# Performance work log

Hardware: AMD Instinct MI355X
Metric: run time of the kernel (lower is better)

## Reference

```python
import jax, jax.numpy as jnp
import numpy as np

Q = 2.0
TEMPERATURE = 1.0
EXP = 1.0 / (Q - 1.0)  # exponent 1/(q-1); q=2 -> sparsemax-style projection
N_BISECT_ITERS = 50    # enough for xtol ~ 1e-6 over an interval of width ~ (u_max - u_min + 10)


def setup_inputs() -> dict:
    key = jax.random.key(0)
    k_x, k_w1, k_w2 = jax.random.split(key, 3)
    B, D, H, E = 8192, 4096, 256, 64
    x = jax.random.normal(k_x, (B, D), dtype=jnp.float32)
    w1 = jax.random.normal(k_w1, (D, H), dtype=jnp.float32) * 0.02
    b1 = jnp.zeros((H,), dtype=jnp.float32)
    w2 = jax.random.normal(k_w2, (H, E), dtype=jnp.float32) * 0.05
    b2 = jnp.zeros((E,), dtype=jnp.float32)
    return {"x": x, "w1": w1, "b1": b1, "w2": w2, "b2": b2}


def _bisect_tau(us):
    # us: [B, E] = utilities / temperature. Find per-row tau with sum(relu(us - tau)**EXP) = 1.
    lo = jnp.min(us, axis=-1) - 10.0   # constraint(lo) > 0
    hi = jnp.max(us, axis=-1)          # constraint(hi) = -1 < 0

    def body(i, carry):
        lo, hi = carry
        mid = 0.5 * (lo + hi)
        f = jnp.sum(jnp.maximum(us - mid[..., None], 0.0) ** EXP, axis=-1) - 1.0
        pos = f > 0.0  # constraint is decreasing in tau: root is above mid
        return (jnp.where(pos, mid, lo), jnp.where(pos, hi, mid))

    lo, hi = jax.lax.fori_loop(0, N_BISECT_ITERS, body, (lo, hi))
    return 0.5 * (lo + hi)  # [B]


def reference(x, w1, b1, w2, b2):
    # utility_net (Dropout is identity in eval mode)
    h = jax.nn.relu(x @ w1 + b1)            # [B, 256]
    utilities = h @ w2 + b2                  # [B, E]
    us = utilities / TEMPERATURE
    # tau is found by root-finding on detached values in the original (.item()),
    # so it is a constant w.r.t. differentiation.
    tau = jax.lax.stop_gradient(_bisect_tau(jax.lax.stop_gradient(us)))
    p = jnp.maximum(us - tau[..., None], 0.0) ** EXP   # [B, E]
    p = p / (jnp.sum(p, axis=-1, keepdims=True) + 1e-8)
    return p
```

## Files before the change

kernel.cpp:

```cpp
#include <hip/hip_runtime.h>
#include <stdint.h>

typedef _Float16 f16;
typedef _Float16 f16x8 __attribute__((ext_vector_type(8)));
typedef float f32x4 __attribute__((ext_vector_type(4)));

#define D_DIM 4096
#define H_DIM 256
#define E_DIM 64
#define BM 128
#define KSPLIT 4
#define NKT2 16
#define HP_SLICE (8192 * 256)

__global__ void pack_kernel(const float* __restrict__ w1, f16* __restrict__ w1s,
                            const float* __restrict__ w2, f16* __restrict__ w2s) {
  const int b = blockIdx.x;
  const int t = threadIdx.x;
  if (b < 512) {
    const int u = b * 256 + t;
    const int lane = u & 63;
    const int kk = (u >> 6) & 1;
    const int c16 = (u >> 7) & 15;
    const int kt = u >> 11;
    const int g = lane >> 4, r = lane & 15;
    const int k0 = kt * 64 + kk * 32 + g * 8;
    const int col = c16 * 16 + r;
    f16x8 o;
#pragma unroll
    for (int j = 0; j < 8; ++j) o[j] = (f16)w1[(size_t)(k0 + j) * H_DIM + col];
    *(f16x8*)(w1s + (size_t)u * 8) = o;
  } else {
    const int u = (b - 512) * 256 + t;
    const int lane = u & 63;
    const int ks = (u >> 6) & 7;
    const int cg = u >> 9;
    const int g = lane >> 4, r = lane & 15;
    const int k0 = ks * 32 + g * 8;
    const int col = cg * 16 + r;
    f16x8 o;
#pragma unroll
    for (int j = 0; j < 8; ++j) o[j] = (f16)w2[(size_t)(k0 + j) * E_DIM + col];
    *(f16x8*)(w2s + (size_t)u * 8) = o;
  }
}

__launch_bounds__(512, 2)
__global__ void gemm1_splitk_kernel(const float* __restrict__ x,
                                    const f16* __restrict__ w1s,
                                    f16* __restrict__ hpart) {
  __shared__ __align__(16) float xbuf[4][BM * 64];

  const int t = threadIdx.x;
  const int lane = t & 63;
  const int wn = t >> 6;
  const int wm = wn >> 2, wc = wn & 3;
  const int g = lane >> 4, r = lane & 15;
  const int bid = blockIdx.x;
  const int ks = bid & 3;
  const int brow = (bid >> 2) * BM;
  const int kph = (bid * 5) & 15;
#define KT(s) ((kph + (s)) & 15)

  const int drow = lane >> 4;
  int hbo[4];
#pragma unroll
  for (int i = 0; i < 4; ++i) hbo[i] = ((lane & 15) ^ ((i * 4 + drow) & 15)) * 4;
  const float* dbase = x + (size_t)(brow + wn * 16 + drow) * D_DIM + ks * 1024;

  const f16* bptr = w1s + (size_t)ks * (16 * 16384) + (size_t)(wc * 8) * 512 + lane * 8;

  f32x4 acc[4][4];
#pragma unroll
  for (int mf = 0; mf < 4; ++mf)
#pragma unroll
    for (int nf = 0; nf < 4; ++nf) acc[mf][nf] = (f32x4){0.f, 0.f, 0.f, 0.f};

  f16x8 BE[8], BO[8];

#define GLDS(bufidx, kt)                                                        \
  {                                                                             \
    _Pragma("unroll") for (int i = 0; i < 4; ++i) {                             \
      const float* gp_ = dbase + (size_t)(i * 4) * D_DIM + (kt) * 64 + hbo[i];  \
      __builtin_amdgcn_global_load_lds(                                         \
          (const __attribute__((address_space(1))) void*)gp_,                   \
          (__attribute__((address_space(3))) void*)&xbuf[bufidx][(wn * 4 + i) * 256], \
          16, 0, 0);                                                            \
    }                                                                           \
  }
#define LDB(kt, B)                                                      \
  {                                                                     \
    const f16* p_ = bptr + (size_t)(kt) * 16384;                        \
    _Pragma("unroll") for (int q = 0; q < 8; ++q)                       \
      (B)[q] = *(const f16x8*)(p_ + q * 512);                           \
  }
#define COMP(bufidx, B)                                                         \
  {                                                                             \
    _Pragma("unroll") for (int kk = 0; kk < 2; ++kk) {                          \
      _Pragma("unroll") for (int mf = 0; mf < 4; ++mf) {                        \
        const int row_ = wm * 64 + mf * 16 + r;                                 \
        const float* bp_ = &xbuf[bufidx][row_ * 64];                            \
        const int L0_ = kk * 8 + g * 2;                                         \
        const float4 a0_ = *(const float4*)(bp_ + ((L0_ ^ r) << 2));            \
        const float4 a1_ = *(const float4*)(bp_ + (((L0_ + 1) ^ r) << 2));      \
        f16x8 af_;                                                              \
        af_[0] = (f16)a0_.x; af_[1] = (f16)a0_.y;                               \
        af_[2] = (f16)a0_.z; af_[3] = (f16)a0_.w;                               \
        af_[4] = (f16)a1_.x; af_[5] = (f16)a1_.y;                               \
        af_[6] = (f16)a1_.z; af_[7] = (f16)a1_.w;                               \
        _Pragma("unroll") for (int nf = 0; nf < 4; ++nf)                        \
          acc[mf][nf] = __builtin_amdgcn_mfma_f32_16x16x32_f16(                 \
              af_, (B)[nf * 2 + kk], acc[mf][nf], 0, 0, 0);                     \
      }                                                                         \
    }                                                                           \
  }
#define STEP(s, bidx, B)                                  \
  {                                                       \
    GLDS(((s) + 2) & 3, KT((s) + 2));                     \
    asm volatile("s_waitcnt vmcnt(16)" ::: "memory");     \
    __builtin_amdgcn_s_barrier();                         \
    COMP(bidx, B);                                        \
    LDB(KT((s) + 2), B);                                  \
  }
#define STEPN(s, bidx, B, WAIT)                           \
  {                                                       \
    asm volatile(WAIT ::: "memory");                      \
    __builtin_amdgcn_s_barrier();                         \
    COMP(bidx, B);                                        \
  }

  GLDS(0, KT(0));
  LDB(KT(0), BE);
  GLDS(1, KT(1));
  LDB(KT(1), BO);

#pragma unroll 1
  for (int q = 0; q < 3; ++q) {
    const int s0 = q * 4;
    STEP(s0 + 0, 0, BE);
    STEP(s0 + 1, 1, BO);
    STEP(s0 + 2, 2, BE);
    STEP(s0 + 3, 3, BO);
  }
  STEP(12, 0, BE);
  STEP(13, 1, BO);
  STEPN(14, 2, BE, "s_waitcnt vmcnt(12)");
  STEPN(15, 3, BO, "s_waitcnt vmcnt(0)");

  f16* hp = hpart + (size_t)ks * HP_SLICE + (size_t)brow * H_DIM;
#pragma unroll
  for (int mf = 0; mf < 4; ++mf)
#pragma unroll
    for (int nf = 0; nf < 4; ++nf) {
      const int col = wc * 64 + nf * 16 + r;
#pragma unroll
      for (int j = 0; j < 4; ++j) {
        const int row = wm * 64 + mf * 16 + g * 4 + j;
        hp[(size_t)row * H_DIM + col] = (f16)acc[mf][nf][j];
      }
    }
}

__launch_bounds__(512)
__global__ void reduce_fused_kernel(const f16* __restrict__ hpart,
                                    const float* __restrict__ b1,
                                    const f16* __restrict__ w2s,
                                    const float* __restrict__ b2,
                                    float* __restrict__ out) {
  __shared__ __align__(16) char smem[24576];
  f16* h_lds = (f16*)smem;
  float* u_lds = (float*)(smem + 16384);

  const int t = threadIdx.x;
  const int lane = t & 63;
  const int wn = t >> 6;
  const int g = lane >> 4, r = lane & 15;
  const int brow = blockIdx.x * 32;

  const int row = t >> 4;
  const int col0 = (t & 15) << 4;
  const f16* base = hpart + (size_t)(brow + row) * H_DIM + col0;
  float a[16];
#pragma unroll
  for (int j = 0; j < 16; ++j) a[j] = 0.f;
#pragma unroll
  for (int c = 0; c < KSPLIT; ++c) {
    const f16x8 va = *(const f16x8*)(base + (size_t)c * HP_SLICE);
    const f16x8 vb = *(const f16x8*)(base + (size_t)c * HP_SLICE + 8);
#pragma unroll
    for (int j = 0; j < 8; ++j) { a[j] += (float)va[j]; a[8 + j] += (float)vb[j]; }
  }
  {
    const int s8 = (row & 7) << 3;
    f16x8 h0, h1;
#pragma unroll
    for (int j = 0; j < 8; ++j) {
      h0[j] = (f16)fmaxf(a[j] + b1[col0 + j], 0.f);
      h1[j] = (f16)fmaxf(a[8 + j] + b1[col0 + 8 + j], 0.f);
    }
    *(f16x8*)(h_lds + row * 256 + (col0 ^ s8)) = h0;
    *(f16x8*)(h_lds + row * 256 + ((col0 + 8) ^ s8)) = h1;
  }
  __syncthreads();

  const int rh2 = wn & 1;
  const int cg = wn >> 1;
  f32x4 acc2 = {0.f, 0.f, 0.f, 0.f};
  const f16* w2p = w2s + (size_t)(cg * 8) * 512 + lane * 8;
#pragma unroll
  for (int ksi = 0; ksi < 8; ++ksi) {
    const int arow = rh2 * 16 + r;
    const int kb = ksi * 32 + g * 8;
    const f16x8 af = *(const f16x8*)(h_lds + arow * 256 + (kb ^ ((arow & 7) << 3)));
    const f16x8 bf = *(const f16x8*)(w2p + ksi * 512);
    acc2 = __builtin_amdgcn_mfma_f32_16x16x32_f16(af, bf, acc2, 0, 0, 0);
  }
  {
    const int col = cg * 16 + r;
    const float bias = b2[col];
#pragma unroll
    for (int j = 0; j < 4; ++j) {
      const int rr = rh2 * 16 + g * 4 + j;
      u_lds[rr * 64 + col] = acc2[j] + bias;
    }
  }
  __syncthreads();

  const int srow = wn * 4 + (lane >> 4);
  const int scol = (lane & 15) << 2;
  const float4 uv = *(const float4*)(u_lds + srow * 64 + scol);
  float u0 = uv.x, u1 = uv.y, u2 = uv.z, u3 = uv.w;

  float mx = fmaxf(fmaxf(u0, u1), fmaxf(u2, u3));
  float mn = fminf(fminf(u0, u1), fminf(u2, u3));
#pragma unroll
  for (int m = 1; m < 16; m <<= 1) {
    mx = fmaxf(mx, __shfl_xor(mx, m));
    mn = fminf(mn, __shfl_xor(mn, m));
  }
  float lo = mn - 10.0f, hi = mx;
#pragma unroll 1
  for (int it = 0; it < 32; ++it) {
    const float mid = 0.5f * (lo + hi);
    float sm = fmaxf(u0 - mid, 0.f) + fmaxf(u1 - mid, 0.f) +
               fmaxf(u2 - mid, 0.f) + fmaxf(u3 - mid, 0.f);
#pragma unroll
    for (int m = 1; m < 16; m <<= 1) sm += __shfl_xor(sm, m);
    const bool pos = (sm - 1.0f) > 0.0f;
    lo = pos ? mid : lo;
    hi = pos ? hi : mid;
  }
  const float tau = 0.5f * (lo + hi);
  const float p0 = fmaxf(u0 - tau, 0.f);
  const float p1 = fmaxf(u1 - tau, 0.f);
  const float p2 = fmaxf(u2 - tau, 0.f);
  const float p3 = fmaxf(u3 - tau, 0.f);
  float sum = p0 + p1 + p2 + p3;
#pragma unroll
  for (int m = 1; m < 16; m <<= 1) sum += __shfl_xor(sum, m);
  const float inv = 1.0f / (sum + 1e-8f);
  float4 pv;
  pv.x = p0 * inv; pv.y = p1 * inv; pv.z = p2 * inv; pv.w = p3 * inv;
  *(float4*)(out + (size_t)(brow + srow) * E_DIM + scol) = pv;
}

extern "C" void kernel_launch(void* const* d_in, const int* in_sizes, int n_in,
                              void* d_out, int out_size, void* d_ws, size_t ws_size,
                              hipStream_t stream) {
  const float* x  = (const float*)d_in[0];
  const float* w1 = (const float*)d_in[1];
  const float* b1 = (const float*)d_in[2];
  const float* w2 = (const float*)d_in[3];
  const float* b2 = (const float*)d_in[4];
  float* out = (float*)d_out;

  char* wsb = (char*)d_ws;
  f16* w1s = (f16*)wsb;
  f16* w2s = (f16*)(wsb + (2u << 20));
  f16* hpart = (f16*)(wsb + (4u << 20));

  pack_kernel<<<520, 256, 0, stream>>>(w1, w1s, w2, w2s);
  gemm1_splitk_kernel<<<256, 512, 0, stream>>>(x, w1s, hpart);
  reduce_fused_kernel<<<256, 512, 0, stream>>>(hpart, b1, w2s, b2, out);
}
```

Baseline: 53.07 us.

## Stage x as fp16 in LDS and DMA W1 tiles into shared double buffers

```diff
diff --git a/kernel.cpp b/kernel.cpp
--- a/kernel.cpp
+++ b/kernel.cpp
@@ -3,6 +3,7 @@
 
 typedef _Float16 f16;
 typedef _Float16 f16x8 __attribute__((ext_vector_type(8)));
+typedef _Float16 f16x4 __attribute__((ext_vector_type(4)));
 typedef float f32x4 __attribute__((ext_vector_type(4)));
 
 #define D_DIM 4096
@@ -45,16 +46,18 @@
   }
 }
 
-__launch_bounds__(512, 2)
+__launch_bounds__(512)
 __global__ void gemm1_splitk_kernel(const float* __restrict__ x,
                                     const f16* __restrict__ w1s,
                                     f16* __restrict__ hpart) {
-  __shared__ __align__(16) float xbuf[4][BM * 64];
+  __shared__ __align__(16) f16 Abuf[2][BM * 64];
+  __shared__ __align__(16) f16 Bbuf[2][16384];
 
   const int t = threadIdx.x;
   const int lane = t & 63;
   const int wn = t >> 6;
-  const int wm = wn >> 2, wc = wn & 3;
+  const int wm = wn >> 2;
+  const int wc = wn & 3;
   const int g = lane >> 4, r = lane & 15;
   const int bid = blockIdx.x;
   const int ks = bid & 3;
@@ -62,13 +65,11 @@
   const int kph = (bid * 5) & 15;
 #define KT(s) ((kph + (s)) & 15)
 
-  const int drow = lane >> 4;
-  int hbo[4];
-#pragma unroll
-  for (int i = 0; i < 4; ++i) hbo[i] = ((lane & 15) ^ ((i * 4 + drow) & 15)) * 4;
-  const float* dbase = x + (size_t)(brow + wn * 16 + drow) * D_DIM + ks * 1024;
-
-  const f16* bptr = w1s + (size_t)ks * (16 * 16384) + (size_t)(wc * 8) * 512 + lane * 8;
+  const float* xb = x + (size_t)(brow + (t >> 4)) * D_DIM + ks * 1024 + ((t & 15) << 2);
+  const int stw_swz = (((t & 15) << 2) ^ (((t >> 4) & 7) << 3));
+  const int stw_row0 = (t >> 4);
+
+  const f16* bsl = w1s + (size_t)ks * (16 * 16384);
 
   f32x4 acc[4][4];
 #pragma unroll
@@ -76,76 +77,68 @@
 #pragma unroll
     for (int nf = 0; nf < 4; ++nf) acc[mf][nf] = (f32x4){0.f, 0.f, 0.f, 0.f};
 
-  f16x8 BE[8], BO[8];
-
-#define GLDS(bufidx, kt)                                                        \
-  {                                                                             \
-    _Pragma("unroll") for (int i = 0; i < 4; ++i) {                             \
-      const float* gp_ = dbase + (size_t)(i * 4) * D_DIM + (kt) * 64 + hbo[i];  \
-      __builtin_amdgcn_global_load_lds(                                         \
-          (const __attribute__((address_space(1))) void*)gp_,                   \
-          (__attribute__((address_space(3))) void*)&xbuf[bufidx][(wn * 4 + i) * 256], \
-          16, 0, 0);                                                            \
-    }                                                                           \
-  }
-#define LDB(kt, B)                                                      \
+  float4 xA[4];
+
+#define LDX(kt)                                                         \
   {                                                                     \
-    const f16* p_ = bptr + (size_t)(kt) * 16384;                        \
-    _Pragma("unroll") for (int q = 0; q < 8; ++q)                       \
-      (B)[q] = *(const f16x8*)(p_ + q * 512);                           \
-  }
-#define COMP(bufidx, B)                                                         \
+    _Pragma("unroll") for (int i = 0; i < 4; ++i)                       \
+      xA[i] = *(const float4*)(xb + (size_t)i * (32 * D_DIM) + (kt) * 64); \
+  }
+#define STW(p)                                                          \
+  {                                                                     \
+    _Pragma("unroll") for (int i = 0; i < 4; ++i) {                     \
+      f16x4 hv_;                                                        \
+      hv_[0] = (f16)xA[i].x; hv_[1] = (f16)xA[i].y;                     \
+      hv_[2] = (f16)xA[i].z; hv_[3] = (f16)xA[i].w;                     \
+      *(f16x4*)(&Abuf[p][(i * 32 + stw_row0) * 64 + stw_swz]) = hv_;    \
+    }                                                                   \
+  }
+#define DMAB(p, kt)                                                     \
+  {                                                                     \
+    _Pragma("unroll") for (int q = 0; q < 4; ++q) {                     \
+      const f16* gs_ = bsl + (size_t)(kt) * 16384 +                     \
+                       (q * 512 + wn * 64 + lane) * 8;                  \
+      __builtin_amdgcn_global_load_lds(                                 \
+          (const __attribute__((address_space(1))) void*)gs_,           \
+          (__attribute__((address_space(3))) void*)                     \
+              (&Bbuf[p][(q * 512 + wn * 64) * 8]),                      \
+          16, 0, 0);                                                    \
+    }                                                                   \
+  }
+#define COMP(p)                                                                 \
   {                                                                             \
     _Pragma("unroll") for (int kk = 0; kk < 2; ++kk) {                          \
+      const int kb_ = (kk * 32 + g * 8) ^ ((r & 7) << 3);                       \
       _Pragma("unroll") for (int mf = 0; mf < 4; ++mf) {                        \
         const int row_ = wm * 64 + mf * 16 + r;                                 \
-        const float* bp_ = &xbuf[bufidx][row_ * 64];                            \
-        const int L0_ = kk * 8 + g * 2;                                         \
-        const float4 a0_ = *(const float4*)(bp_ + ((L0_ ^ r) << 2));            \
-        const float4 a1_ = *(const float4*)(bp_ + (((L0_ + 1) ^ r) << 2));      \
-        f16x8 af_;                                                              \
-        af_[0] = (f16)a0_.x; af_[1] = (f16)a0_.y;                               \
-        af_[2] = (f16)a0_.z; af_[3] = (f16)a0_.w;                               \
-        af_[4] = (f16)a1_.x; af_[5] = (f16)a1_.y;                               \
-        af_[6] = (f16)a1_.z; af_[7] = (f16)a1_.w;                               \
-        _Pragma("unroll") for (int nf = 0; nf < 4; ++nf)                        \
+        const f16x8 af_ = *(const f16x8*)(&Abuf[p][row_ * 64 + kb_]);           \
+        _Pragma("unroll") for (int nf = 0; nf < 4; ++nf) {                      \
+          const f16x8 bf_ =                                                     \
+              *(const f16x8*)(&Bbuf[p][(wc * 8 + nf * 2 + kk) * 512 + lane * 8]); \
           acc[mf][nf] = __builtin_amdgcn_mfma_f32_16x16x32_f16(                 \
-              af_, (B)[nf * 2 + kk], acc[mf][nf], 0, 0, 0);                     \
+              af_, bf_, acc[mf][nf], 0, 0, 0);                                  \
+        }                                                                       \
       }                                                                         \
     }                                                                           \
   }
-#define STEP(s, bidx, B)                                  \
-  {                                                       \
-    GLDS(((s) + 2) & 3, KT((s) + 2));                     \
-    asm volatile("s_waitcnt vmcnt(16)" ::: "memory");     \
-    __builtin_amdgcn_s_barrier();                         \
-    COMP(bidx, B);                                        \
-    LDB(KT((s) + 2), B);                                  \
-  }
-#define STEPN(s, bidx, B, WAIT)                           \
-  {                                                       \
-    asm volatile(WAIT ::: "memory");                      \
-    __builtin_amdgcn_s_barrier();                         \
-    COMP(bidx, B);                                        \
-  }
-
-  GLDS(0, KT(0));
-  LDB(KT(0), BE);
-  GLDS(1, KT(1));
-  LDB(KT(1), BO);
+
+  DMAB(0, KT(0));
+  LDX(KT(0));
+  STW(0);
+  LDX(KT(1));
+  __syncthreads();
 
 #pragma unroll 1
-  for (int q = 0; q < 3; ++q) {
-    const int s0 = q * 4;
-    STEP(s0 + 0, 0, BE);
-    STEP(s0 + 1, 1, BO);
-    STEP(s0 + 2, 2, BE);
-    STEP(s0 + 3, 3, BO);
-  }
-  STEP(12, 0, BE);
-  STEP(13, 1, BO);
-  STEPN(14, 2, BE, "s_waitcnt vmcnt(12)");
-  STEPN(15, 3, BO, "s_waitcnt vmcnt(0)");
+  for (int s = 0; s < NKT2; ++s) {
+    const int p = s & 1;
+    if (s + 1 < NKT2) {
+      DMAB(p ^ 1, KT(s + 1));
+      STW(p ^ 1);
+      if (s + 2 < NKT2) LDX(KT(s + 2));
+    }
+    COMP(p);
+    __syncthreads();
+  }
 
   f16* hp = hpart + (size_t)ks * HP_SLICE + (size_t)brow * H_DIM;
 #pragma unroll
```

Result: slower. 56.78 us (+7.0%).

## Fuse pack, split-K GEMM and reduce into one cooperative kernel

Applied to the files above, without the earlier changes.

```diff
diff --git a/kernel.cpp b/kernel.cpp
--- a/kernel.cpp
+++ b/kernel.cpp
@@ -3,6 +3,7 @@
 
 typedef _Float16 f16;
 typedef _Float16 f16x8 __attribute__((ext_vector_type(8)));
+typedef _Float16 f16x4 __attribute__((ext_vector_type(4)));
 typedef float f32x4 __attribute__((ext_vector_type(4)));
 
 #define D_DIM 4096
@@ -12,71 +13,91 @@
 #define KSPLIT 4
 #define NKT2 16
 #define HP_SLICE (8192 * 256)
-
-__global__ void pack_kernel(const float* __restrict__ w1, f16* __restrict__ w1s,
-                            const float* __restrict__ w2, f16* __restrict__ w2s) {
-  const int b = blockIdx.x;
+#define NBLK 256
+
+__device__ __forceinline__ void grid_barrier(unsigned* ctr, unsigned nb) {
+  __syncthreads();
+  if (threadIdx.x == 0) {
+    __threadfence();
+    __hip_atomic_fetch_add(ctr, 1u, __ATOMIC_RELEASE, __HIP_MEMORY_SCOPE_AGENT);
+    while (__hip_atomic_load(ctr, __ATOMIC_ACQUIRE, __HIP_MEMORY_SCOPE_AGENT) < nb)
+      __builtin_amdgcn_s_sleep(2);
+    __threadfence();
+  }
+  __syncthreads();
+}
+
+__launch_bounds__(512)
+__global__ void coop_kernel(const float* __restrict__ x,
+                            const float* __restrict__ w1,
+                            const float* __restrict__ b1,
+                            const float* __restrict__ w2,
+                            const float* __restrict__ b2,
+                            f16* __restrict__ w1s, f16* __restrict__ w2s,
+                            f16* __restrict__ hpart, unsigned* __restrict__ bar,
+                            float* __restrict__ out) {
+  __shared__ __align__(16) char smem[131072];
+
+  const int bid = blockIdx.x;
   const int t = threadIdx.x;
-  if (b < 512) {
-    const int u = b * 256 + t;
-    const int lane = u & 63;
+  const int lane = t & 63;
+  const int wn = t >> 6;
+  const int g = lane >> 4, r = lane & 15;
+
+  {
+    const int u = bid * 512 + t;
+    const int plane = u & 63;
     const int kk = (u >> 6) & 1;
     const int c16 = (u >> 7) & 15;
     const int kt = u >> 11;
-    const int g = lane >> 4, r = lane & 15;
-    const int k0 = kt * 64 + kk * 32 + g * 8;
-    const int col = c16 * 16 + r;
+    const int pg = plane >> 4, pr = plane & 15;
+    const int k0 = kt * 64 + kk * 32 + pg * 8;
+    const int col = c16 * 16 + pr;
     f16x8 o;
 #pragma unroll
     for (int j = 0; j < 8; ++j) o[j] = (f16)w1[(size_t)(k0 + j) * H_DIM + col];
     *(f16x8*)(w1s + (size_t)u * 8) = o;
-  } else {
-    const int u = (b - 512) * 256 + t;
-    const int lane = u & 63;
-    const int ks = (u >> 6) & 7;
-    const int cg = u >> 9;
-    const int g = lane >> 4, r = lane & 15;
-    const int k0 = ks * 32 + g * 8;
-    const int col = cg * 16 + r;
-    f16x8 o;
-#pragma unroll
-    for (int j = 0; j < 8; ++j) o[j] = (f16)w2[(size_t)(k0 + j) * E_DIM + col];
-    *(f16x8*)(w2s + (size_t)u * 8) = o;
-  }
-}
-
-__launch_bounds__(512, 2)
-__global__ void gemm1_splitk_kernel(const float* __restrict__ x,
-                                    const f16* __restrict__ w1s,
-                                    f16* __restrict__ hpart) {
-  __shared__ __align__(16) float xbuf[4][BM * 64];
-
-  const int t = threadIdx.x;
-  const int lane = t & 63;
-  const int wn = t >> 6;
-  const int wm = wn >> 2, wc = wn & 3;
-  const int g = lane >> 4, r = lane & 15;
-  const int bid = blockIdx.x;
-  const int ks = bid & 3;
-  const int brow = (bid >> 2) * BM;
+    if (bid < 4) {
+      const int u2 = bid * 512 + t;
+      const int l2 = u2 & 63;
+      const int ks2 = (u2 >> 6) & 7;
+      const int cg2 = u2 >> 9;
+      const int g2 = l2 >> 4, r2 = l2 & 15;
+      const int k02 = ks2 * 32 + g2 * 8;
+      const int col2 = cg2 * 16 + r2;
+      f16x8 o2;
+#pragma unroll
+      for (int j = 0; j < 8; ++j) o2[j] = (f16)w2[(size_t)(k02 + j) * E_DIM + col2];
+      *(f16x8*)(w2s + (size_t)u2 * 8) = o2;
+    }
+  }
+  grid_barrier(bar + 0, NBLK);
+
+  const int xcd = bid & 7;
+  const int idx = bid >> 3;
+  const int ks = idx >> 3;
+  const int rb = xcd + 8 * (idx & 7);
+  const int brow = rb * BM;
   const int kph = (bid * 5) & 15;
 #define KT(s) ((kph + (s)) & 15)
 
-  const int drow = lane >> 4;
-  int hbo[4];
-#pragma unroll
-  for (int i = 0; i < 4; ++i) hbo[i] = ((lane & 15) ^ ((i * 4 + drow) & 15)) * 4;
-  const float* dbase = x + (size_t)(brow + wn * 16 + drow) * D_DIM + ks * 1024;
-
-  const f16* bptr = w1s + (size_t)ks * (16 * 16384) + (size_t)(wc * 8) * 512 + lane * 8;
-
-  f32x4 acc[4][4];
-#pragma unroll
-  for (int mf = 0; mf < 4; ++mf)
-#pragma unroll
-    for (int nf = 0; nf < 4; ++nf) acc[mf][nf] = (f32x4){0.f, 0.f, 0.f, 0.f};
-
-  f16x8 BE[8], BO[8];
+  {
+    float* xbuf = (float*)smem;
+    const int wm = wn >> 2, wc = wn & 3;
+
+    const int drow = lane >> 4;
+    int hbo[4];
+#pragma unroll
+    for (int i = 0; i < 4; ++i) hbo[i] = ((lane & 15) ^ ((i * 4 + drow) & 15)) * 4;
+    const float* dbase = x + (size_t)(brow + wn * 16 + drow) * D_DIM + ks * 1024;
+    const f16* bptr = w1s + (size_t)ks * (16 * 16384) + (size_t)(wc * 8) * 512 + lane * 8;
+
+    f32x4 acc[4][4];
+#pragma unroll
+    for (int mf = 0; mf < 4; ++mf)
+#pragma unroll
+      for (int nf = 0; nf < 4; ++nf) acc[mf][nf] = (f32x4){0.f, 0.f, 0.f, 0.f};
+    f16x8 BE[8], BO[8];
 
 #define GLDS(bufidx, kt)                                                        \
   {                                                                             \
@@ -84,7 +105,8 @@
       const float* gp_ = dbase + (size_t)(i * 4) * D_DIM + (kt) * 64 + hbo[i];  \
       __builtin_amdgcn_global_load_lds(                                         \
           (const __attribute__((address_space(1))) void*)gp_,                   \
-          (__attribute__((address_space(3))) void*)&xbuf[bufidx][(wn * 4 + i) * 256], \
+          (__attribute__((address_space(3))) void*)                             \
+              (xbuf + (bufidx) * (BM * 64) + (wn * 4 + i) * 256),               \
           16, 0, 0);                                                            \
     }                                                                           \
   }
@@ -99,7 +121,7 @@
     _Pragma("unroll") for (int kk = 0; kk < 2; ++kk) {                          \
       _Pragma("unroll") for (int mf = 0; mf < 4; ++mf) {                        \
         const int row_ = wm * 64 + mf * 16 + r;                                 \
-        const float* bp_ = &xbuf[bufidx][row_ * 64];                            \
+        const float* bp_ = xbuf + (bufidx) * (BM * 64) + row_ * 64;             \
         const int L0_ = kk * 8 + g * 2;                                         \
         const float4 a0_ = *(const float4*)(bp_ + ((L0_ ^ r) << 2));            \
         const float4 a1_ = *(const float4*)(bp_ + (((L0_ + 1) ^ r) << 2));      \
@@ -129,139 +151,133 @@
     COMP(bidx, B);                                        \
   }
 
-  GLDS(0, KT(0));
-  LDB(KT(0), BE);
-  GLDS(1, KT(1));
-  LDB(KT(1), BO);
+    GLDS(0, KT(0));
+    LDB(KT(0), BE);
+    GLDS(1, KT(1));
+    LDB(KT(1), BO);
 
 #pragma unroll 1
-  for (int q = 0; q < 3; ++q) {
-    const int s0 = q * 4;
-    STEP(s0 + 0, 0, BE);
-    STEP(s0 + 1, 1, BO);
-    STEP(s0 + 2, 2, BE);
-    STEP(s0 + 3, 3, BO);
-  }
-  STEP(12, 0, BE);
-  STEP(13, 1, BO);
-  STEPN(14, 2, BE, "s_waitcnt vmcnt(12)");
-  STEPN(15, 3, BO, "s_waitcnt vmcnt(0)");
-
-  f16* hp = hpart + (size_t)ks * HP_SLICE + (size_t)brow * H_DIM;
-#pragma unroll
-  for (int mf = 0; mf < 4; ++mf)
-#pragma unroll
-    for (int nf = 0; nf < 4; ++nf) {
-      const int col = wc * 64 + nf * 16 + r;
+    for (int q = 0; q < 3; ++q) {
+      const int s0 = q * 4;
+      STEP(s0 + 0, 0, BE);
+      STEP(s0 + 1, 1, BO);
+      STEP(s0 + 2, 2, BE);
+      STEP(s0 + 3, 3, BO);
+    }
+    STEP(12, 0, BE);
+    STEP(13, 1, BO);
+    STEPN(14, 2, BE, "s_waitcnt vmcnt(12)");
+    STEPN(15, 3, BO, "s_waitcnt vmcnt(0)");
+
+    f16* hp = hpart + (size_t)ks * HP_SLICE + (size_t)brow * H_DIM;
+#pragma unroll
+    for (int mf = 0; mf < 4; ++mf)
+#pragma unroll
+      for (int nf = 0; nf < 4; ++nf) {
+        const int col = wc * 64 + nf * 16 + r;
+#pragma unroll
+        for (int j = 0; j < 4; ++j) {
+          const int row = wm * 64 + mf * 16 + g * 4 + j;
+          hp[(size_t)row * H_DIM + col] = (f16)acc[mf][nf][j];
+        }
+      }
+  }
+  grid_barrier(bar + 16, NBLK);
+
+  {
+    f16* h_lds = (f16*)smem;
+    float* u_lds = (float*)(smem + 16384);
+    const int idx2 = bid >> 3;
+    const int rb2 = xcd + 8 * (idx2 & 7);
+    const int sub = idx2 >> 3;
+    const int brow2 = rb2 * 128 + sub * 32;
+
+    const int row = t >> 4;
+    const int col0 = (t & 15) << 4;
+    const f16* base = hpart + (size_t)(brow2 + row) * H_DIM + col0;
+    float a[16];
+#pragma unroll
+    for (int j = 0; j < 16; ++j) a[j] = 0.f;
+#pragma unroll
+    for (int c = 0; c < KSPLIT; ++c) {
+      const f16x8 va = *(const f16x8*)(base + (size_t)c * HP_SLICE);
+      const f16x8 vb = *(const f16x8*)(base + (size_t)c * HP_SLICE + 8);
+#pragma unroll
+      for (int j = 0; j < 8; ++j) { a[j] += (float)va[j]; a[8 + j] += (float)vb[j]; }
+    }
+    {
+      const int s8 = (row & 7) << 3;
+      f16x8 h0, h1;
+#pragma unroll
+      for (int j = 0; j < 8; ++j) {
+        h0[j] = (f16)fmaxf(a[j] + b1[col0 + j], 0.f);
+        h1[j] = (f16)fmaxf(a[8 + j] + b1[col0 + 8 + j], 0.f);
+      }
+      *(f16x8*)(h_lds + row * 256 + (col0 ^ s8)) = h0;
+      *(f16x8*)(h_lds + row * 256 + ((col0 + 8) ^ s8)) = h1;
+    }
+    __syncthreads();
+
+    const int rh2 = wn & 1;
+    const int cg = wn >> 1;
+    f32x4 acc2 = {0.f, 0.f, 0.f, 0.f};
+    const f16* w2p = w2s + (size_t)(cg * 8) * 512 + lane * 8;
+#pragma unroll
+    for (int ksi = 0; ksi < 8; ++ksi) {
+      const int arow = rh2 * 16 + r;
+      const int kb = ksi * 32 + g * 8;
+      const f16x8 af = *(const f16x8*)(h_lds + arow * 256 + (kb ^ ((arow & 7) << 3)));
+      const f16x8 bf = *(const f16x8*)(w2p + ksi * 512);
+      acc2 = __builtin_amdgcn_mfma_f32_16x16x32_f16(af, bf, acc2, 0, 0, 0);
+    }
+    {
+      const int col = cg * 16 + r;
+      const float bias = b2[col];
 #pragma unroll
       for (int j = 0; j < 4; ++j) {
-        const int row = wm * 64 + mf * 16 + g * 4 + j;
-        hp[(size_t)row * H_DIM + col] = (f16)acc[mf][nf][j];
+        const int rr = rh2 * 16 + g * 4 + j;
+        u_lds[rr * 64 + col] = acc2[j] + bias;
       }
     }
-}
-
-__launch_bounds__(512)
-__global__ void reduce_fused_kernel(const f16* __restrict__ hpart,
-                                    const float* __restrict__ b1,
-                                    const f16* __restrict__ w2s,
-                                    const float* __restrict__ b2,
-                                    float* __restrict__ out) {
-  __shared__ __align__(16) char smem[24576];
-  f16* h_lds = (f16*)smem;
-  float* u_lds = (float*)(smem + 16384);
-
-  const int t = threadIdx.x;
-  const int lane = t & 63;
-  const int wn = t >> 6;
-  const int g = lane >> 4, r = lane & 15;
-  const int brow = blockIdx.x * 32;
-
-  const int row = t >> 4;
-  const int col0 = (t & 15) << 4;
-  const f16* base = hpart + (size_t)(brow + row) * H_DIM + col0;
-  float a[16];
-#pragma unroll
-  for (int j = 0; j < 16; ++j) a[j] = 0.f;
-#pragma unroll
-  for (int c = 0; c < KSPLIT; ++c) {
-    const f16x8 va = *(const f16x8*)(base + (size_t)c * HP_SLICE);
-    const f16x8 vb = *(const f16x8*)(base + (size_t)c * HP_SLICE + 8);
-#pragma unroll
-    for (int j = 0; j < 8; ++j) { a[j] += (float)va[j]; a[8 + j] += (float)vb[j]; }
-  }
-  {
-    const int s8 = (row & 7) << 3;
-    f16x8 h0, h1;
-#pragma unroll
-    for (int j = 0; j < 8; ++j) {
-      h0[j] = (f16)fmaxf(a[j] + b1[col0 + j], 0.f);
-      h1[j] = (f16)fmaxf(a[8 + j] + b1[col0 + 8 + j], 0.f);
-    }
-    *(f16x8*)(h_lds + row * 256 + (col0 ^ s8)) = h0;
-    *(f16x8*)(h_lds + row * 256 + ((col0 + 8) ^ s8)) = h1;
-  }
-  __syncthreads();
-
-  const int rh2 = wn & 1;
-  const int cg = wn >> 1;
-  f32x4 acc2 = {0.f, 0.f, 0.f, 0.f};
-  const f16* w2p = w2s + (size_t)(cg * 8) * 512 + lane * 8;
-#pragma unroll
-  for (int ksi = 0; ksi < 8; ++ksi) {
-    const int arow = rh2 * 16 + r;
-    const int kb = ksi * 32 + g * 8;
-    const f16x8 af = *(const f16x8*)(h_lds + arow * 256 + (kb ^ ((arow & 7) << 3)));
-    const f16x8 bf = *(const f16x8*)(w2p + ksi * 512);
-    acc2 = __builtin_amdgcn_mfma_f32_16x16x32_f16(af, bf, acc2, 0, 0, 0);
-  }
-  {
-    const int col = cg * 16 + r;
-    const float bias = b2[col];
-#pragma unroll
-    for (int j = 0; j < 4; ++j) {
-      const int rr = rh2 * 16 + g * 4 + j;
-      u_lds[rr * 64 + col] = acc2[j] + bias;
-    }
-  }
-  __syncthreads();
-
-  const int srow = wn * 4 + (lane >> 4);
-  const int scol = (lane & 15) << 2;
-  const float4 uv = *(const float4*)(u_lds + srow * 64 + scol);
-  float u0 = uv.x, u1 = uv.y, u2 = uv.z, u3 = uv.w;
-
-  float mx = fmaxf(fmaxf(u0, u1), fmaxf(u2, u3));
-  float mn = fminf(fminf(u0, u1), fminf(u2, u3));
-#pragma unroll
-  for (int m = 1; m < 16; m <<= 1) {
-    mx = fmaxf(mx, __shfl_xor(mx, m));
-    mn = fminf(mn, __shfl_xor(mn, m));
-  }
-  float lo = mn - 10.0f, hi = mx;
+    __syncthreads();
+
+    const int srow = wn * 4 + (lane >> 4);
+    const int scol = (lane & 15) << 2;
+    const float4 uv = *(const float4*)(u_lds + srow * 64 + scol);
+    float u0 = uv.x, u1 = uv.y, u2 = uv.z, u3 = uv.w;
+
+    float mx = fmaxf(fmaxf(u0, u1), fmaxf(u2, u3));
+    float mn = fminf(fminf(u0, u1), fminf(u2, u3));
+#pragma unroll
+    for (int m = 1; m < 16; m <<= 1) {
+      mx = fmaxf(mx, __shfl_xor(mx, m));
+      mn = fminf(mn, __shfl_xor(mn, m));
+    }
+    float lo = mn - 10.0f, hi = mx;
 #pragma unroll 1
-  for (int it = 0; it < 32; ++it) {
-    const float mid = 0.5f * (lo + hi);
-    float sm = fmaxf(u0 - mid, 0.f) + fmaxf(u1 - mid, 0.f) +
-               fmaxf(u2 - mid, 0.f) + fmaxf(u3 - mid, 0.f);
-#pragma unroll
-    for (int m = 1; m < 16; m <<= 1) sm += __shfl_xor(sm, m);
-    const bool pos = (sm - 1.0f) > 0.0f;
-    lo = pos ? mid : lo;
-    hi = pos ? hi : mid;
-  }
-  const float tau = 0.5f * (lo + hi);
-  const float p0 = fmaxf(u0 - tau, 0.f);
-  const float p1 = fmaxf(u1 - tau, 0.f);
-  const float p2 = fmaxf(u2 - tau, 0.f);
-  const float p3 = fmaxf(u3 - tau, 0.f);
-  float sum = p0 + p1 + p2 + p3;
-#pragma unroll
-  for (int m = 1; m < 16; m <<= 1) sum += __shfl_xor(sum, m);
-  const float inv = 1.0f / (sum + 1e-8f);
-  float4 pv;
-  pv.x = p0 * inv; pv.y = p1 * inv; pv.z = p2 * inv; pv.w = p3 * inv;
-  *(float4*)(out + (size_t)(brow + srow) * E_DIM + scol) = pv;
+    for (int it = 0; it < 32; ++it) {
+      const float mid = 0.5f * (lo + hi);
+      float sm = fmaxf(u0 - mid, 0.f) + fmaxf(u1 - mid, 0.f) +
+                 fmaxf(u2 - mid, 0.f) + fmaxf(u3 - mid, 0.f);
+#pragma unroll
+      for (int m = 1; m < 16; m <<= 1) sm += __shfl_xor(sm, m);
+      const bool pos = (sm - 1.0f) > 0.0f;
+      lo = pos ? mid : lo;
+      hi = pos ? hi : mid;
+    }
+    const float tau = 0.5f * (lo + hi);
+    const float p0 = fmaxf(u0 - tau, 0.f);
+    const float p1 = fmaxf(u1 - tau, 0.f);
+    const float p2 = fmaxf(u2 - tau, 0.f);
+    const float p3 = fmaxf(u3 - tau, 0.f);
+    float sum = p0 + p1 + p2 + p3;
+#pragma unroll
+    for (int m = 1; m < 16; m <<= 1) sum += __shfl_xor(sum, m);
+    const float inv = 1.0f / (sum + 1e-8f);
+    float4 pv;
+    pv.x = p0 * inv; pv.y = p1 * inv; pv.z = p2 * inv; pv.w = p3 * inv;
+    *(float4*)(out + (size_t)(brow2 + srow) * E_DIM + scol) = pv;
+  }
 }
 
 extern "C" void kernel_launch(void* const* d_in, const int* in_sizes, int n_in,
@@ -278,8 +294,12 @@
   f16* w1s = (f16*)wsb;
   f16* w2s = (f16*)(wsb + (2u << 20));
   f16* hpart = (f16*)(wsb + (4u << 20));
-
-  pack_kernel<<<520, 256, 0, stream>>>(w1, w1s, w2, w2s);
-  gemm1_splitk_kernel<<<256, 512, 0, stream>>>(x, w1s, hpart);
-  reduce_fused_kernel<<<256, 512, 0, stream>>>(hpart, b1, w2s, b2, out);
+  unsigned* bar = (unsigned*)(wsb + (20u << 20));
+
+  hipMemsetAsync(bar, 0, 128, stream);
+
+  void* args[] = {(void*)&x, (void*)&w1, (void*)&b1, (void*)&w2, (void*)&b2,
+                  (void*)&w1s, (void*)&w2s, (void*)&hpart, (void*)&bar, (void*)&out};
+  hipLaunchCooperativeKernel((const void*)coop_kernel, dim3(NBLK), dim3(512),
+                             args, 0, stream);
 }
```

New measurement: 141.3 us. +166.2%, slower.

## Fuse split-K reduction and epilogue into GEMM1 via last-block atomic counter

Applied to the files above, without the earlier changes.

```diff
diff --git a/kernel.cpp b/kernel.cpp
--- a/kernel.cpp
+++ b/kernel.cpp
@@ -3,6 +3,7 @@
 
 typedef _Float16 f16;
 typedef _Float16 f16x8 __attribute__((ext_vector_type(8)));
+typedef _Float16 f16x4 __attribute__((ext_vector_type(4)));
 typedef float f32x4 __attribute__((ext_vector_type(4)));
 
 #define D_DIM 4096
@@ -45,11 +46,17 @@
   }
 }
 
-__launch_bounds__(512, 2)
-__global__ void gemm1_splitk_kernel(const float* __restrict__ x,
-                                    const f16* __restrict__ w1s,
-                                    f16* __restrict__ hpart) {
-  __shared__ __align__(16) float xbuf[4][BM * 64];
+__launch_bounds__(512)
+__global__ void gemm1_fused_kernel(const float* __restrict__ x,
+                                   const f16* __restrict__ w1s,
+                                   const float* __restrict__ b1,
+                                   const f16* __restrict__ w2s,
+                                   const float* __restrict__ b2,
+                                   f16* __restrict__ hpart,
+                                   unsigned* __restrict__ cnt,
+                                   float* __restrict__ out) {
+  __shared__ __align__(16) char smem[131072];
+  __shared__ unsigned last_flag;
 
   const int t = threadIdx.x;
   const int lane = t & 63;
@@ -58,16 +65,18 @@
   const int g = lane >> 4, r = lane & 15;
   const int bid = blockIdx.x;
   const int ks = bid & 3;
-  const int brow = (bid >> 2) * BM;
+  const int rb = bid >> 2;
+  const int brow = rb * BM;
   const int kph = (bid * 5) & 15;
 #define KT(s) ((kph + (s)) & 15)
 
+  float* xbuf = (float*)smem;
+
   const int drow = lane >> 4;
   int hbo[4];
 #pragma unroll
   for (int i = 0; i < 4; ++i) hbo[i] = ((lane & 15) ^ ((i * 4 + drow) & 15)) * 4;
   const float* dbase = x + (size_t)(brow + wn * 16 + drow) * D_DIM + ks * 1024;
-
   const f16* bptr = w1s + (size_t)ks * (16 * 16384) + (size_t)(wc * 8) * 512 + lane * 8;
 
   f32x4 acc[4][4];
@@ -75,7 +84,6 @@
   for (int mf = 0; mf < 4; ++mf)
 #pragma unroll
     for (int nf = 0; nf < 4; ++nf) acc[mf][nf] = (f32x4){0.f, 0.f, 0.f, 0.f};
-
   f16x8 BE[8], BO[8];
 
 #define GLDS(bufidx, kt)                                                        \
@@ -84,7 +92,8 @@
       const float* gp_ = dbase + (size_t)(i * 4) * D_DIM + (kt) * 64 + hbo[i];  \
       __builtin_amdgcn_global_load_lds(                                         \
           (const __attribute__((address_space(1))) void*)gp_,                   \
-          (__attribute__((address_space(3))) void*)&xbuf[bufidx][(wn * 4 + i) * 256], \
+          (__attribute__((address_space(3))) void*)                             \
+              (xbuf + (bufidx) * (BM * 64) + (wn * 4 + i) * 256),               \
           16, 0, 0);                                                            \
     }                                                                           \
   }
@@ -99,7 +108,7 @@
     _Pragma("unroll") for (int kk = 0; kk < 2; ++kk) {                          \
       _Pragma("unroll") for (int mf = 0; mf < 4; ++mf) {                        \
         const int row_ = wm * 64 + mf * 16 + r;                                 \
-        const float* bp_ = &xbuf[bufidx][row_ * 64];                            \
+        const float* bp_ = xbuf + (bufidx) * (BM * 64) + row_ * 64;             \
         const int L0_ = kk * 8 + g * 2;                                         \
         const float4 a0_ = *(const float4*)(bp_ + ((L0_ ^ r) << 2));            \
         const float4 a1_ = *(const float4*)(bp_ + (((L0_ + 1) ^ r) << 2));      \
@@ -147,121 +156,123 @@
   STEPN(14, 2, BE, "s_waitcnt vmcnt(12)");
   STEPN(15, 3, BO, "s_waitcnt vmcnt(0)");
 
-  f16* hp = hpart + (size_t)ks * HP_SLICE + (size_t)brow * H_DIM;
-#pragma unroll
-  for (int mf = 0; mf < 4; ++mf)
-#pragma unroll
-    for (int nf = 0; nf < 4; ++nf) {
-      const int col = wc * 64 + nf * 16 + r;
-#pragma unroll
-      for (int j = 0; j < 4; ++j) {
-        const int row = wm * 64 + mf * 16 + g * 4 + j;
-        hp[(size_t)row * H_DIM + col] = (f16)acc[mf][nf][j];
-      }
-    }
-}
-
-__launch_bounds__(512)
-__global__ void reduce_fused_kernel(const f16* __restrict__ hpart,
-                                    const float* __restrict__ b1,
-                                    const f16* __restrict__ w2s,
-                                    const float* __restrict__ b2,
-                                    float* __restrict__ out) {
-  __shared__ __align__(16) char smem[24576];
+  {
+    f16* hp = hpart + (size_t)ks * HP_SLICE + (size_t)brow * H_DIM;
+#pragma unroll
+    for (int mf = 0; mf < 4; ++mf)
+#pragma unroll
+      for (int nf = 0; nf < 4; ++nf) {
+        const int col = wc * 64 + nf * 16 + r;
+#pragma unroll
+        for (int j = 0; j < 4; ++j) {
+          const int row = wm * 64 + mf * 16 + g * 4 + j;
+          hp[(size_t)row * H_DIM + col] = (f16)acc[mf][nf][j];
+        }
+      }
+  }
+
+  asm volatile("s_waitcnt vmcnt(0)" ::: "memory");
+  __syncthreads();
+  if (t == 0) {
+    last_flag = __hip_atomic_fetch_add(&cnt[rb], 1u, __ATOMIC_ACQ_REL,
+                                       __HIP_MEMORY_SCOPE_AGENT);
+  }
+  __syncthreads();
+  if (last_flag != KSPLIT - 1) return;
+
   f16* h_lds = (f16*)smem;
   float* u_lds = (float*)(smem + 16384);
 
-  const int t = threadIdx.x;
-  const int lane = t & 63;
-  const int wn = t >> 6;
-  const int g = lane >> 4, r = lane & 15;
-  const int brow = blockIdx.x * 32;
-
-  const int row = t >> 4;
-  const int col0 = (t & 15) << 4;
-  const f16* base = hpart + (size_t)(brow + row) * H_DIM + col0;
-  float a[16];
-#pragma unroll
-  for (int j = 0; j < 16; ++j) a[j] = 0.f;
-#pragma unroll
-  for (int c = 0; c < KSPLIT; ++c) {
-    const f16x8 va = *(const f16x8*)(base + (size_t)c * HP_SLICE);
-    const f16x8 vb = *(const f16x8*)(base + (size_t)c * HP_SLICE + 8);
-#pragma unroll
-    for (int j = 0; j < 8; ++j) { a[j] += (float)va[j]; a[8 + j] += (float)vb[j]; }
-  }
-  {
-    const int s8 = (row & 7) << 3;
-    f16x8 h0, h1;
-#pragma unroll
-    for (int j = 0; j < 8; ++j) {
-      h0[j] = (f16)fmaxf(a[j] + b1[col0 + j], 0.f);
-      h1[j] = (f16)fmaxf(a[8 + j] + b1[col0 + 8 + j], 0.f);
-    }
-    *(f16x8*)(h_lds + row * 256 + (col0 ^ s8)) = h0;
-    *(f16x8*)(h_lds + row * 256 + ((col0 + 8) ^ s8)) = h1;
-  }
-  __syncthreads();
-
-  const int rh2 = wn & 1;
-  const int cg = wn >> 1;
-  f32x4 acc2 = {0.f, 0.f, 0.f, 0.f};
-  const f16* w2p = w2s + (size_t)(cg * 8) * 512 + lane * 8;
-#pragma unroll
-  for (int ksi = 0; ksi < 8; ++ksi) {
-    const int arow = rh2 * 16 + r;
-    const int kb = ksi * 32 + g * 8;
-    const f16x8 af = *(const f16x8*)(h_lds + arow * 256 + (kb ^ ((arow & 7) << 3)));
-    const f16x8 bf = *(const f16x8*)(w2p + ksi * 512);
-    acc2 = __builtin_amdgcn_mfma_f32_16x16x32_f16(af, bf, acc2, 0, 0, 0);
-  }
-  {
-    const int col = cg * 16 + r;
-    const float bias = b2[col];
-#pragma unroll
-    for (int j = 0; j < 4; ++j) {
-      const int rr = rh2 * 16 + g * 4 + j;
-      u_lds[rr * 64 + col] = acc2[j] + bias;
-    }
-  }
-  __syncthreads();
-
-  const int srow = wn * 4 + (lane >> 4);
-  const int scol = (lane & 15) << 2;
-  const float4 uv = *(const float4*)(u_lds + srow * 64 + scol);
-  float u0 = uv.x, u1 = uv.y, u2 = uv.z, u3 = uv.w;
-
-  float mx = fmaxf(fmaxf(u0, u1), fmaxf(u2, u3));
-  float mn = fminf(fminf(u0, u1), fminf(u2, u3));
-#pragma unroll
-  for (int m = 1; m < 16; m <<= 1) {
-    mx = fmaxf(mx, __shfl_xor(mx, m));
-    mn = fminf(mn, __shfl_xor(mn, m));
-  }
-  float lo = mn - 10.0f, hi = mx;
 #pragma unroll 1
-  for (int it = 0; it < 32; ++it) {
-    const float mid = 0.5f * (lo + hi);
-    float sm = fmaxf(u0 - mid, 0.f) + fmaxf(u1 - mid, 0.f) +
-               fmaxf(u2 - mid, 0.f) + fmaxf(u3 - mid, 0.f);
-#pragma unroll
-    for (int m = 1; m < 16; m <<= 1) sm += __shfl_xor(sm, m);
-    const bool pos = (sm - 1.0f) > 0.0f;
-    lo = pos ? mid : lo;
-    hi = pos ? hi : mid;
-  }
-  const float tau = 0.5f * (lo + hi);
-  const float p0 = fmaxf(u0 - tau, 0.f);
-  const float p1 = fmaxf(u1 - tau, 0.f);
-  const float p2 = fmaxf(u2 - tau, 0.f);
-  const float p3 = fmaxf(u3 - tau, 0.f);
-  float sum = p0 + p1 + p2 + p3;
-#pragma unroll
-  for (int m = 1; m < 16; m <<= 1) sum += __shfl_xor(sum, m);
-  const float inv = 1.0f / (sum + 1e-8f);
-  float4 pv;
-  pv.x = p0 * inv; pv.y = p1 * inv; pv.z = p2 * inv; pv.w = p3 * inv;
-  *(float4*)(out + (size_t)(brow + srow) * E_DIM + scol) = pv;
+  for (int sub = 0; sub < 4; ++sub) {
+    const int brow2 = brow + sub * 32;
+    __syncthreads();
+    {
+      const int row = t >> 4;
+      const int col0 = (t & 15) << 4;
+      const f16* base = hpart + (size_t)(brow2 + row) * H_DIM + col0;
+      float a[16];
+#pragma unroll
+      for (int j = 0; j < 16; ++j) a[j] = 0.f;
+#pragma unroll
+      for (int c = 0; c < KSPLIT; ++c) {
+        const f16x8 va = *(const f16x8*)(base + (size_t)c * HP_SLICE);
+        const f16x8 vb = *(const f16x8*)(base + (size_t)c * HP_SLICE + 8);
+#pragma unroll
+        for (int j = 0; j < 8; ++j) { a[j] += (float)va[j]; a[8 + j] += (float)vb[j]; }
+      }
+      const int s8 = (row & 7) << 3;
+      f16x8 h0, h1;
+#pragma unroll
+      for (int j = 0; j < 8; ++j) {
+        h0[j] = (f16)fmaxf(a[j] + b1[col0 + j], 0.f);
+        h1[j] = (f16)fmaxf(a[8 + j] + b1[col0 + 8 + j], 0.f);
+      }
+      *(f16x8*)(h_lds + row * 256 + (col0 ^ s8)) = h0;
+      *(f16x8*)(h_lds + row * 256 + ((col0 + 8) ^ s8)) = h1;
+    }
+    __syncthreads();
+
+    const int rh2 = wn & 1;
+    const int cg = wn >> 1;
+    f32x4 acc2 = {0.f, 0.f, 0.f, 0.f};
+    const f16* w2p = w2s + (size_t)(cg * 8) * 512 + lane * 8;
+#pragma unroll
+    for (int ksi = 0; ksi < 8; ++ksi) {
+      const int arow = rh2 * 16 + r;
+      const int kb = ksi * 32 + g * 8;
+      const f16x8 af = *(const f16x8*)(h_lds + arow * 256 + (kb ^ ((arow & 7) << 3)));
+      const f16x8 bf = *(const f16x8*)(w2p + ksi * 512);
+      acc2 = __builtin_amdgcn_mfma_f32_16x16x32_f16(af, bf, acc2, 0, 0, 0);
+    }
+    {
+      const int col = cg * 16 + r;
+      const float bias = b2[col];
+#pragma unroll
+      for (int j = 0; j < 4; ++j) {
+        const int rr = rh2 * 16 + g * 4 + j;
+        u_lds[rr * 64 + col] = acc2[j] + bias;
+      }
+    }
+    __syncthreads();
+
+    const int srow = wn * 4 + (lane >> 4);
+    const int scol = (lane & 15) << 2;
+    const float4 uv = *(const float4*)(u_lds + srow * 64 + scol);
+    float u0 = uv.x, u1 = uv.y, u2 = uv.z, u3 = uv.w;
+
+    float mx = fmaxf(fmaxf(u0, u1), fmaxf(u2, u3));
+    float mn = fminf(fminf(u0, u1), fminf(u2, u3));
+#pragma unroll
+    for (int m = 1; m < 16; m <<= 1) {
+      mx = fmaxf(mx, __shfl_xor(mx, m));
+      mn = fminf(mn, __shfl_xor(mn, m));
+    }
+    float lo = mn - 10.0f, hi = mx;
+#pragma unroll 1
+    for (int it = 0; it < 32; ++it) {
+      const float mid = 0.5f * (lo + hi);
+      float sm = fmaxf(u0 - mid, 0.f) + fmaxf(u1 - mid, 0.f) +
+                 fmaxf(u2 - mid, 0.f) + fmaxf(u3 - mid, 0.f);
+#pragma unroll
+      for (int m = 1; m < 16; m <<= 1) sm += __shfl_xor(sm, m);
+      const bool pos = (sm - 1.0f) > 0.0f;
+      lo = pos ? mid : lo;
+      hi = pos ? hi : mid;
+    }
+    const float tau = 0.5f * (lo + hi);
+    const float p0 = fmaxf(u0 - tau, 0.f);
+    const float p1 = fmaxf(u1 - tau, 0.f);
+    const float p2 = fmaxf(u2 - tau, 0.f);
+    const float p3 = fmaxf(u3 - tau, 0.f);
+    float sum = p0 + p1 + p2 + p3;
+#pragma unroll
+    for (int m = 1; m < 16; m <<= 1) sum += __shfl_xor(sum, m);
+    const float inv = 1.0f / (sum + 1e-8f);
+    float4 pv;
+    pv.x = p0 * inv; pv.y = p1 * inv; pv.z = p2 * inv; pv.w = p3 * inv;
+    *(float4*)(out + (size_t)(brow2 + srow) * E_DIM + scol) = pv;
+  }
 }
 
 extern "C" void kernel_launch(void* const* d_in, const int* in_sizes, int n_in,
@@ -278,8 +289,9 @@
   f16* w1s = (f16*)wsb;
   f16* w2s = (f16*)(wsb + (2u << 20));
   f16* hpart = (f16*)(wsb + (4u << 20));
-
+  unsigned* cnt = (unsigned*)(wsb + (20u << 20));
+
+  hipMemsetAsync(cnt, 0, 64 * sizeof(unsigned), stream);
   pack_kernel<<<520, 256, 0, stream>>>(w1, w1s, w2, w2s);
-  gemm1_splitk_kernel<<<256, 512, 0, stream>>>(x, w1s, hpart);
-  reduce_fused_kernel<<<256, 512, 0, stream>>>(hpart, b1, w2s, b2, out);
+  gemm1_fused_kernel<<<256, 512, 0, stream>>>(x, w1s, b1, w2s, b2, hpart, cnt, out);
 }
```

Result: slower. 85.85 us (+61.8%).
